# Optimization experiments

Hardware: AMD Instinct MI355X
Metric: run time of the kernel (lower is better)

## Reference

```python
import jax, jax.numpy as jnp
import numpy as np

N = 4096
IN_DIM, HID, OUT_DIM = 512, 256, 64
PROP_STEP = 10
LAM_HAT = 0.9
SCAD_A = 3.7
EPS = 1e-8


def setup_inputs() -> dict:
    key = jax.random.key(0)
    kA, kF, k1, k2 = jax.random.split(key, 4)
    # sparse symmetric 0/1 adjacency, zero diagonal (add_loops adds I later)
    u = jax.random.uniform(kA, (N, N), dtype=jnp.float32)
    A = (u < 0.005).astype(jnp.float32)
    A = jnp.maximum(A, A.T)
    A = A * (1.0 - jnp.eye(N, dtype=jnp.float32))
    F = jax.random.normal(kF, (N, IN_DIM), dtype=jnp.float32)
    W1 = jax.random.normal(k1, (IN_DIM, HID), dtype=jnp.float32) / np.sqrt(IN_DIM)
    b1 = jnp.zeros((HID,), dtype=jnp.float32)
    W2 = jax.random.normal(k2, (HID, OUT_DIM), dtype=jnp.float32) / np.sqrt(HID)
    b2 = jnp.zeros((OUT_DIM,), dtype=jnp.float32)
    raw_gamma = jnp.zeros((PROP_STEP,), dtype=jnp.float32)
    return {"A": A, "F": F, "W1": W1, "b1": b1, "W2": W2, "b2": b2,
            "raw_gamma": raw_gamma}


def reference(A, F, W1, b1, W2, b2, raw_gamma):
    lam = 1.0 / LAM_HAT - 1.0
    a = SCAD_A
    # MLP (dropout inactive at inference)
    F0 = jax.nn.relu(F @ W1 + b1) @ W2 + b2            # [N, out_dim]
    eye = jnp.eye(A.shape[0], dtype=A.dtype)
    A = A + eye                                        # add_loops
    D = A.sum(-1)                                      # [N]
    D_sq = jnp.sqrt(D)[:, None]                        # [N, 1]
    A_tilde = A / D_sq / D_sq.T                        # sym_norm: D^-1/2 A D^-1/2
    gammas = jax.nn.sigmoid(raw_gamma) * 2.0           # per-layer gamma in (0, 2)

    def step(Fc, gamma_k):
        Fn = Fc / D_sq
        nrm = jnp.linalg.norm(Fn, axis=-1, keepdims=True)
        Fu = Fn / jnp.maximum(nrm, 1e-12)
        # cosine distance in [0, 2]; detached as in torch (.detach())
        y = jax.lax.stop_gradient(1.0 - Fu @ Fu.T)     # [N, N]
        lam_k = jnp.maximum(gamma_k / a, EPS)
        t = a * lam_k
        safe_y = jnp.where(y <= 0.0, 1.0, y)
        w_mid = (t - y) / ((a - 1.0) * safe_y)
        # SCAD weight: 1 for y<=lam_k, linear decay on [lam_k, a*lam_k], 0 beyond
        W = jnp.where(y <= lam_k, 1.0, jnp.where(y <= t, w_mid, 0.0))
        W = W * (1.0 - eye)
        W = jnp.where(jnp.isnan(W), 1.0, W)
        Q_hat = ((W * A).sum(-1) / D + lam)[:, None]   # [N, 1]
        F_new = (W * A_tilde) @ Fc / Q_hat + lam * F0 / Q_hat
        return F_new, None

    F_out, _ = jax.lax.scan(step, F0, gammas)
    return F_out
```

## Files before the change

kernel.cpp:

```cpp
#include <hip/hip_runtime.h>
#include <hip/hip_bf16.h>

#define N_NODES 4096
#define IN_DIM  512
#define HID_DIM 256
#define OUT_DIM 64
#define PROP_STEP 10
#define MAX_DEG 128
#define GEMM_BLOCKS 256
#define SCAN_BLOCKS 512
#define LAM_CONST (1.0f/0.9f - 1.0f)
#define SCAD_A 3.7f

__device__ __forceinline__ ushort f2bf(float f) {
    unsigned u = __float_as_uint(f);
    unsigned r = (u + 0x7FFFu + ((u >> 16) & 1u)) >> 16;
    return (ushort)r;
}
__device__ __forceinline__ unsigned pack2(float lo, float hi) {
    return (unsigned)f2bf(lo) | ((unsigned)f2bf(hi) << 16);
}
__device__ __forceinline__ float bflo(unsigned u) { return __uint_as_float(u << 16); }
__device__ __forceinline__ float bfhi(unsigned u) { return __uint_as_float(u & 0xFFFF0000u); }
__device__ __forceinline__ float4 f4add(float4 a, float4 b) {
    return make_float4(a.x + b.x, a.y + b.y, a.z + b.z, a.w + b.w);
}

#define FMA16(AV, WV) \
    acc0.x = fmaf(AV.x, WV.x, acc0.x); acc0.y = fmaf(AV.x, WV.y, acc0.y); \
    acc0.z = fmaf(AV.x, WV.z, acc0.z); acc0.w = fmaf(AV.x, WV.w, acc0.w); \
    acc1.x = fmaf(AV.y, WV.x, acc1.x); acc1.y = fmaf(AV.y, WV.y, acc1.y); \
    acc1.z = fmaf(AV.y, WV.z, acc1.z); acc1.w = fmaf(AV.y, WV.w, acc1.w); \
    acc2.x = fmaf(AV.z, WV.x, acc2.x); acc2.y = fmaf(AV.z, WV.y, acc2.y); \
    acc2.z = fmaf(AV.z, WV.z, acc2.z); acc2.w = fmaf(AV.z, WV.w, acc2.w); \
    acc3.x = fmaf(AV.w, WV.x, acc3.x); acc3.y = fmaf(AV.w, WV.y, acc3.y); \
    acc3.z = fmaf(AV.w, WV.z, acc3.z); acc3.w = fmaf(AV.w, WV.w, acc3.w);

#define STEP(KK, WV) { float4 a_ = *(const float4*)&sF[(KK) * 16 + rg4]; FMA16(a_, WV); }

#define P2ROW(HV, PV) \
    PV.x = fmaf(HV.x, w0.x, PV.x); PV.y = fmaf(HV.x, w0.y, PV.y); \
    PV.z = fmaf(HV.x, w0.z, PV.z); PV.w = fmaf(HV.x, w0.w, PV.w); \
    PV.x = fmaf(HV.y, w1.x, PV.x); PV.y = fmaf(HV.y, w1.y, PV.y); \
    PV.z = fmaf(HV.y, w1.z, PV.z); PV.w = fmaf(HV.y, w1.w, PV.w); \
    PV.x = fmaf(HV.z, w2.x, PV.x); PV.y = fmaf(HV.z, w2.y, PV.y); \
    PV.z = fmaf(HV.z, w2.z, PV.z); PV.w = fmaf(HV.z, w2.w, PV.w); \
    PV.x = fmaf(HV.w, w3.x, PV.x); PV.y = fmaf(HV.w, w3.y, PV.y); \
    PV.z = fmaf(HV.w, w3.z, PV.z); PV.w = fmaf(HV.w, w3.w, PV.w);

__global__ __launch_bounds__(256, 4) void build_all(
    const float* __restrict__ A, const float* __restrict__ F,
    const float* __restrict__ W1, const float* __restrict__ b1,
    const float* __restrict__ W2, const float* __restrict__ b2,
    float* __restrict__ F0,
    int* __restrict__ ell, int* __restrict__ deg,
    float* __restrict__ invD, float* __restrict__ invDsq)
{
    __shared__ float smem[8192];
    if (blockIdx.x >= SCAN_BLOCKS) {
        float* sF = smem;
        int t  = threadIdx.x;
        int m0 = (blockIdx.x - SCAN_BLOCKS) * 16;
        {
            int r = t & 15, kc = (t >> 4) * 32;
            const float* src = F + (size_t)(m0 + r) * IN_DIM + kc;
#pragma unroll
            for (int j = 0; j < 8; j++) {
                float4 v = *(const float4*)(src + j * 4);
                sF[(kc + j * 4 + 0) * 16 + r] = v.x;
                sF[(kc + j * 4 + 1) * 16 + r] = v.y;
                sF[(kc + j * 4 + 2) * 16 + r] = v.z;
                sF[(kc + j * 4 + 3) * 16 + r] = v.w;
            }
        }
        __syncthreads();
        int rg4 = (t >> 6) * 4;
        int cg  = t & 63;
        const float* Wp = W1 + cg * 4;
        float4 acc0 = {0,0,0,0}, acc1 = {0,0,0,0}, acc2 = {0,0,0,0}, acc3 = {0,0,0,0};
        float4 wa0 = *(const float4*)(Wp + 0 * HID_DIM);
        float4 wa1 = *(const float4*)(Wp + 1 * HID_DIM);
        float4 wa2 = *(const float4*)(Wp + 2 * HID_DIM);
        float4 wa3 = *(const float4*)(Wp + 3 * HID_DIM);
        float4 wb0 = *(const float4*)(Wp + 4 * HID_DIM);
        float4 wb1 = *(const float4*)(Wp + 5 * HID_DIM);
        float4 wb2 = *(const float4*)(Wp + 6 * HID_DIM);
        float4 wb3 = *(const float4*)(Wp + 7 * HID_DIM);
        for (int kb = 0; kb < IN_DIM; kb += 8) {
            STEP(kb + 0, wa0) STEP(kb + 1, wa1) STEP(kb + 2, wa2) STEP(kb + 3, wa3)
            if (kb + 8 < IN_DIM) {
                const float* wn = Wp + (size_t)(kb + 8) * HID_DIM;
                wa0 = *(const float4*)(wn);
                wa1 = *(const float4*)(wn + HID_DIM);
                wa2 = *(const float4*)(wn + 2 * HID_DIM);
                wa3 = *(const float4*)(wn + 3 * HID_DIM);
            }
            STEP(kb + 4, wb0) STEP(kb + 5, wb1) STEP(kb + 6, wb2) STEP(kb + 7, wb3)
            if (kb + 8 < IN_DIM) {
                const float* wn = Wp + (size_t)(kb + 12) * HID_DIM;
                wb0 = *(const float4*)(wn);
                wb1 = *(const float4*)(wn + HID_DIM);
                wb2 = *(const float4*)(wn + 2 * HID_DIM);
                wb3 = *(const float4*)(wn + 3 * HID_DIM);
            }
        }
        __syncthreads();
        float* sH   = smem;
        float* sRed = smem + 4096;
        {
            float4 bv = *(const float4*)(b1 + cg * 4);
            float4 h0 = make_float4(fmaxf(acc0.x + bv.x, 0.f), fmaxf(acc0.y + bv.y, 0.f),
                                    fmaxf(acc0.z + bv.z, 0.f), fmaxf(acc0.w + bv.w, 0.f));
            float4 h1 = make_float4(fmaxf(acc1.x + bv.x, 0.f), fmaxf(acc1.y + bv.y, 0.f),
                                    fmaxf(acc1.z + bv.z, 0.f), fmaxf(acc1.w + bv.w, 0.f));
            float4 h2 = make_float4(fmaxf(acc2.x + bv.x, 0.f), fmaxf(acc2.y + bv.y, 0.f),
                                    fmaxf(acc2.z + bv.z, 0.f), fmaxf(acc2.w + bv.w, 0.f));
            float4 h3 = make_float4(fmaxf(acc3.x + bv.x, 0.f), fmaxf(acc3.y + bv.y, 0.f),
                                    fmaxf(acc3.z + bv.z, 0.f), fmaxf(acc3.w + bv.w, 0.f));
            *(float4*)&sH[(rg4 + 0) * 256 + cg * 4] = h0;
            *(float4*)&sH[(rg4 + 1) * 256 + cg * 4] = h1;
            *(float4*)&sH[(rg4 + 2) * 256 + cg * 4] = h2;
            *(float4*)&sH[(rg4 + 3) * 256 + cg * 4] = h3;
        }
        __syncthreads();
        int lane = t & 63, wid = t >> 6;
        int rgrp = lane >> 4;
        int cg2  = lane & 15;
        float4 p0 = {0,0,0,0}, p1 = {0,0,0,0}, p2 = {0,0,0,0}, p3 = {0,0,0,0};
        int kbase = wid * 64;
        for (int kq = 0; kq < 64; kq += 4) {
            int kg = kbase + kq;
            float4 h0 = *(const float4*)&sH[(rgrp * 4 + 0) * 256 + kg];
            float4 h1 = *(const float4*)&sH[(rgrp * 4 + 1) * 256 + kg];
            float4 h2 = *(const float4*)&sH[(rgrp * 4 + 2) * 256 + kg];
            float4 h3 = *(const float4*)&sH[(rgrp * 4 + 3) * 256 + kg];
            float4 w0 = *(const float4*)(W2 + (size_t)(kg + 0) * OUT_DIM + cg2 * 4);
            float4 w1 = *(const float4*)(W2 + (size_t)(kg + 1) * OUT_DIM + cg2 * 4);
            float4 w2 = *(const float4*)(W2 + (size_t)(kg + 2) * OUT_DIM + cg2 * 4);
            float4 w3 = *(const float4*)(W2 + (size_t)(kg + 3) * OUT_DIM + cg2 * 4);
            P2ROW(h0, p0) P2ROW(h1, p1) P2ROW(h2, p2) P2ROW(h3, p3)
        }
        __syncthreads();
        if (wid) {
            float* dst = sRed + (size_t)(wid - 1) * 1024 + lane * 16;
            *(float4*)(dst + 0)  = p0; *(float4*)(dst + 4)  = p1;
            *(float4*)(dst + 8)  = p2; *(float4*)(dst + 12) = p3;
        }
        __syncthreads();
        if (wid == 0) {
#pragma unroll
            for (int w = 0; w < 3; w++) {
                const float* s = sRed + (size_t)w * 1024 + lane * 16;
                p0 = f4add(p0, *(const float4*)(s + 0));
                p1 = f4add(p1, *(const float4*)(s + 4));
                p2 = f4add(p2, *(const float4*)(s + 8));
                p3 = f4add(p3, *(const float4*)(s + 12));
            }
            float4 b2v = *(const float4*)(b2 + cg2 * 4);
            float* o = F0 + (size_t)(m0 + rgrp * 4) * OUT_DIM + cg2 * 4;
            *(float4*)(o + 0 * OUT_DIM) = f4add(p0, b2v);
            *(float4*)(o + 1 * OUT_DIM) = f4add(p1, b2v);
            *(float4*)(o + 2 * OUT_DIM) = f4add(p2, b2v);
            *(float4*)(o + 3 * OUT_DIM) = f4add(p3, b2v);
        }
    } else {
        int sb   = blockIdx.x;
        int lane = threadIdx.x & 63;
        int wid  = threadIdx.x >> 6;
        int w    = sb * 4 + wid;
        for (int rr = 0; rr < 2; rr++) {
            int row = w * 2 + rr;
            const float* Arow = A + (size_t)row * N_NODES;
            float4 ch[16];
#pragma unroll
            for (int c = 0; c < 16; c++)
                ch[c] = *(const float4*)(Arow + c * 256 + lane * 4);
            int* rdst = ell + (size_t)row * MAX_DEG;
            unsigned cnt = 0;
#pragma unroll
            for (int c = 0; c < 16; c++) {
                float4 v = ch[c];
                int colbase = c * 256 + lane * 4;
#pragma unroll
                for (int q = 0; q < 4; q++) {
                    float vv = (q == 0) ? v.x : (q == 1) ? v.y : (q == 2) ? v.z : v.w;
                    bool nz = (vv != 0.0f);
                    unsigned long long m = __ballot(nz);
                    unsigned rank = __builtin_amdgcn_mbcnt_hi(
                        (unsigned)(m >> 32),
                        __builtin_amdgcn_mbcnt_lo((unsigned)m, 0u));
                    unsigned pos = cnt + rank;
                    if (nz && pos < MAX_DEG) rdst[pos] = colbase + q;
                    cnt += (unsigned)__popcll(m);
                }
            }
            int c  = (cnt > MAX_DEG) ? MAX_DEG : (int)cnt;
            int pad = (c + 15) & ~15;
            if (pad > MAX_DEG) pad = MAX_DEG;
            if (lane >= c && lane < pad) rdst[lane] = row;
            int l2 = lane + 64;
            if (l2 >= c && l2 < pad) rdst[l2] = row;
            if (lane == 0) {
                deg[row] = c;
                float d = (float)(cnt + 1);
                invD[row] = 1.0f / d;
                invDsq[row] = rsqrtf(d);
            }
        }
    }
}

__global__ __launch_bounds__(256, 4) void propagate_f0(
    const float* __restrict__ F0,
    const int* __restrict__ ell, const int* __restrict__ deg,
    const float* __restrict__ invD, const float* __restrict__ invDsq,
    const float* __restrict__ raw_gamma,
    unsigned* __restrict__ Pout, float* __restrict__ nrmOut)
{
    int lane = threadIdx.x & 63;
    int wid  = threadIdx.x >> 6;
    int r    = __builtin_amdgcn_readfirstlane(blockIdx.x * 4 + wid);
    int g    = lane >> 3;
    int sl   = lane & 7;
    const float inv_am1 = 1.0f / (SCAD_A - 1.0f);

    float gamma = 2.0f / (1.0f + expf(-raw_gamma[0]));
    float lam_k = fmaxf(gamma / SCAD_A, 1e-8f);
    float tt    = SCAD_A * lam_k;

    int dg = deg[r];
    int pad = (dg + 15) & ~15;
    int npair = pad >> 4;
    const int* nb = ell + (size_t)r * MAX_DEG;
    int ed0 = (lane < pad)      ? nb[lane]      : r;
    int ed1 = (64 + lane < pad) ? nb[64 + lane] : r;

    float iDs = invDsq[r];
    const float4* f04 = (const float4*)(F0 + (size_t)r * OUT_DIM + sl * 8);
    float4 fa = f04[0], fb = f04[1];
    float f0v[8] = { fa.x, fa.y, fa.z, fa.w, fb.x, fb.y, fb.z, fb.w };
    float ui[8];
    float ssr = 0.0f;
#pragma unroll
    for (int q = 0; q < 8; q++) { ui[q] = f0v[q] * iDs; ssr += ui[q] * ui[q]; }
    ssr += __shfl_xor(ssr, 1, 64);
    ssr += __shfl_xor(ssr, 2, 64);
    ssr += __shfl_xor(ssr, 4, 64);
    float inv_nr = 1.0f / fmaxf(sqrtf(ssr), 1e-12f);
#pragma unroll
    for (int q = 0; q < 8; q++) ui[q] *= inv_nr;

    float acc[8] = {};
    float qsum = 0.0f;
    for (int it = 0; it < npair; ++it) {
        int e0 = it * 16 + g, e1 = e0 + 8;
        int src = (it < 4) ? ed0 : ed1;
        int j0 = __shfl(src, e0 & 63, 64);
        int j1 = __shfl(src, e1 & 63, 64);
        const float4* p0 = (const float4*)(F0 + (size_t)j0 * OUT_DIM + sl * 8);
        const float4* p1 = (const float4*)(F0 + (size_t)j1 * OUT_DIM + sl * 8);
        float4 x0 = p0[0], x1 = p0[1];
        float4 y0 = p1[0], y1 = p1[1];
        float d0 = invDsq[j0], d1 = invDsq[j1];
        float v0[8] = { x0.x*d0, x0.y*d0, x0.z*d0, x0.w*d0, x1.x*d0, x1.y*d0, x1.z*d0, x1.w*d0 };
        float v1[8] = { y0.x*d1, y0.y*d1, y0.z*d1, y0.w*d1, y1.x*d1, y1.y*d1, y1.z*d1, y1.w*d1 };
        float pa = 0.f, pb = 0.f, s0 = 0.f, s1 = 0.f;
#pragma unroll
        for (int q = 0; q < 8; q++) {
            pa += ui[q] * v0[q]; s0 += v0[q] * v0[q];
            pb += ui[q] * v1[q]; s1 += v1[q] * v1[q];
        }
        pa += __shfl_xor(pa, 1, 64); pb += __shfl_xor(pb, 1, 64);
        s0 += __shfl_xor(s0, 1, 64); s1 += __shfl_xor(s1, 1, 64);
        pa += __shfl_xor(pa, 2, 64); pb += __shfl_xor(pb, 2, 64);
        s0 += __shfl_xor(s0, 2, 64); s1 += __shfl_xor(s1, 2, 64);
        pa += __shfl_xor(pa, 4, 64); pb += __shfl_xor(pb, 4, 64);
        s0 += __shfl_xor(s0, 4, 64); s1 += __shfl_xor(s1, 4, 64);
        float n0 = fmaxf(sqrtf(s0), 1e-12f);
        float n1 = fmaxf(sqrtf(s1), 1e-12f);
        float ya = 1.0f - pa / n0, yb = 1.0f - pb / n1;
        float wa = (ya <= lam_k) ? 1.0f : ((ya <= tt) ? (tt - ya) * inv_am1 / ya : 0.0f);
        float wb = (yb <= lam_k) ? 1.0f : ((yb <= tt) ? (tt - yb) * inv_am1 / yb : 0.0f);
        if (e0 >= dg) wa = 0.0f;
        if (e1 >= dg) wb = 0.0f;
        qsum += wa + wb;
#pragma unroll
        for (int q = 0; q < 8; q++) acc[q] += wa * v0[q] + wb * v1[q];
    }

#pragma unroll
    for (int off = 8; off <= 32; off <<= 1) {
#pragma unroll
        for (int q = 0; q < 8; q++) acc[q] += __shfl_xor(acc[q], off, 64);
        qsum += __shfl_xor(qsum, off, 64);
    }

    float Qh  = qsum * invD[r] + LAM_CONST;
    float rQh = 1.0f / Qh;
    float res[8], fn[8];
    float ssq = 0.0f;
#pragma unroll
    for (int q = 0; q < 8; q++) {
        res[q] = (acc[q] * iDs + LAM_CONST * f0v[q]) * rQh;
        fn[q]  = res[q] * iDs;
        ssq   += fn[q] * fn[q];
    }
    ssq += __shfl_xor(ssq, 1, 64);
    ssq += __shfl_xor(ssq, 2, 64);
    ssq += __shfl_xor(ssq, 4, 64);
    float nrm = fmaxf(sqrtf(ssq), 1e-12f);
    float inv_n = 1.0f / nrm;
    if (lane < 8) {
        uint4 fuPk;
        fuPk.x = pack2(fn[0] * inv_n, fn[1] * inv_n);
        fuPk.y = pack2(fn[2] * inv_n, fn[3] * inv_n);
        fuPk.z = pack2(fn[4] * inv_n, fn[5] * inv_n);
        fuPk.w = pack2(fn[6] * inv_n, fn[7] * inv_n);
        *(uint4*)(Pout + (size_t)r * 32 + sl * 4) = fuPk;
    }
    if (lane == 0) nrmOut[r] = nrm;
}

__global__ __launch_bounds__(256, 4) void propagate(
    const unsigned* __restrict__ Pin, const float* __restrict__ nrmIn,
    const float* __restrict__ F0,
    const int* __restrict__ ell, const int* __restrict__ deg,
    const float* __restrict__ invD, const float* __restrict__ invDsq,
    const float* __restrict__ raw_gamma, int step,
    unsigned* __restrict__ Pout, float* __restrict__ nrmOut,
    float* __restrict__ FcOut, int writeNext, int writeOut)
{
    int lane = threadIdx.x & 63;
    int wid  = threadIdx.x >> 6;
    int r    = __builtin_amdgcn_readfirstlane(blockIdx.x * 4 + wid);
    int g    = lane >> 3;
    int sl   = lane & 7;
    const float inv_am1 = 1.0f / (SCAD_A - 1.0f);

    float gamma = 2.0f / (1.0f + expf(-raw_gamma[step]));
    float lam_k = fmaxf(gamma / SCAD_A, 1e-8f);
    float tt    = SCAD_A * lam_k;

    int dg = deg[r];
    int pad = (dg + 15) & ~15;
    int npair = pad >> 4;
    const int* nb = ell + (size_t)r * MAX_DEG;
    int ed0 = (lane < pad)      ? nb[lane]      : r;
    int ed1 = (64 + lane < pad) ? nb[64 + lane] : r;

    uint4 up = *(const uint4*)(Pin + (size_t)r * 32 + sl * 4);
    float ui[8] = { bflo(up.x), bfhi(up.x), bflo(up.y), bfhi(up.y),
                    bflo(up.z), bfhi(up.z), bflo(up.w), bfhi(up.w) };

    float acc[8] = {};
    float qsum = 0.0f;

    auto eidx = [&](int it_, int& J0, int& J1) {
        int e0_ = it_ * 16 + g;
        int src = (it_ < 4) ? ed0 : ed1;
        J0 = __shfl(src, e0_ & 63, 64);
        J1 = __shfl(src, (e0_ + 8) & 63, 64);
    };
    auto body = [&](int it_, uint4 U0, uint4 U1, float NR0, float NR1) {
        float pa = ui[0] * bflo(U0.x) + ui[1] * bfhi(U0.x) + ui[2] * bflo(U0.y) + ui[3] * bfhi(U0.y)
                 + ui[4] * bflo(U0.z) + ui[5] * bfhi(U0.z) + ui[6] * bflo(U0.w) + ui[7] * bfhi(U0.w);
        float pb = ui[0] * bflo(U1.x) + ui[1] * bfhi(U1.x) + ui[2] * bflo(U1.y) + ui[3] * bfhi(U1.y)
                 + ui[4] * bflo(U1.z) + ui[5] * bfhi(U1.z) + ui[6] * bflo(U1.w) + ui[7] * bfhi(U1.w);
        pa += __shfl_xor(pa, 1, 64); pb += __shfl_xor(pb, 1, 64);
        pa += __shfl_xor(pa, 2, 64); pb += __shfl_xor(pb, 2, 64);
        pa += __shfl_xor(pa, 4, 64); pb += __shfl_xor(pb, 4, 64);
        float ya = 1.0f - pa, yb = 1.0f - pb;
        float wa = (ya <= lam_k) ? 1.0f : ((ya <= tt) ? (tt - ya) * inv_am1 / ya : 0.0f);
        float wb = (yb <= lam_k) ? 1.0f : ((yb <= tt) ? (tt - yb) * inv_am1 / yb : 0.0f);
        int e0_ = it_ * 16 + g;
        if (e0_ >= dg)     wa = 0.0f;
        if (e0_ + 8 >= dg) wb = 0.0f;
        qsum += wa + wb;
        float wsa = wa * NR0;
        float wsb = wb * NR1;
        acc[0] += wsa * bflo(U0.x) + wsb * bflo(U1.x);
        acc[1] += wsa * bfhi(U0.x) + wsb * bfhi(U1.x);
        acc[2] += wsa * bflo(U0.y) + wsb * bflo(U1.y);
        acc[3] += wsa * bfhi(U0.y) + wsb * bfhi(U1.y);
        acc[4] += wsa * bflo(U0.z) + wsb * bflo(U1.z);
        acc[5] += wsa * bfhi(U0.z) + wsb * bfhi(U1.z);
        acc[6] += wsa * bflo(U0.w) + wsb * bflo(U1.w);
        acc[7] += wsa * bfhi(U0.w) + wsb * bfhi(U1.w);
    };

    if (npair > 0) {
        uint4 uA0, uA1, uB0, uB1;
        float nA0, nA1, nB0, nB1;
        int j0, j1;
        eidx(0, j0, j1);
        uA0 = *(const uint4*)(Pin + (size_t)j0 * 32 + sl * 4);
        uA1 = *(const uint4*)(Pin + (size_t)j1 * 32 + sl * 4);
        nA0 = nrmIn[j0]; nA1 = nrmIn[j1];
        int it = 0;
        while (true) {
            if (it + 1 < npair) {
                eidx(it + 1, j0, j1);
                uB0 = *(const uint4*)(Pin + (size_t)j0 * 32 + sl * 4);
                uB1 = *(const uint4*)(Pin + (size_t)j1 * 32 + sl * 4);
                nB0 = nrmIn[j0]; nB1 = nrmIn[j1];
            }
            body(it, uA0, uA1, nA0, nA1);
            ++it; if (it >= npair) break;
            if (it + 1 < npair) {
                eidx(it + 1, j0, j1);
                uA0 = *(const uint4*)(Pin + (size_t)j0 * 32 + sl * 4);
                uA1 = *(const uint4*)(Pin + (size_t)j1 * 32 + sl * 4);
                nA0 = nrmIn[j0]; nA1 = nrmIn[j1];
            }
            body(it, uB0, uB1, nB0, nB1);
            ++it; if (it >= npair) break;
        }
    }

#pragma unroll
    for (int off = 8; off <= 32; off <<= 1) {
#pragma unroll
        for (int q = 0; q < 8; q++) acc[q] += __shfl_xor(acc[q], off, 64);
        qsum += __shfl_xor(qsum, off, 64);
    }

    float iDs = invDsq[r];
    float Qh  = qsum * invD[r] + LAM_CONST;
    float rQh = 1.0f / Qh;
    const float4* f04 = (const float4*)(F0 + (size_t)r * OUT_DIM + sl * 8);
    float4 f0a = f04[0], f0b = f04[1];
    float f0v[8] = { f0a.x, f0a.y, f0a.z, f0a.w, f0b.x, f0b.y, f0b.z, f0b.w };
    float res[8];
#pragma unroll
    for (int q = 0; q < 8; q++) res[q] = (acc[q] * iDs + LAM_CONST * f0v[q]) * rQh;

    if (writeOut && lane < 8) {
        float4* o4 = (float4*)(FcOut + (size_t)r * OUT_DIM + sl * 8);
        o4[0] = make_float4(res[0], res[1], res[2], res[3]);
        o4[1] = make_float4(res[4], res[5], res[6], res[7]);
    }
    if (writeNext) {
        float fn[8];
        float ssq = 0.0f;
#pragma unroll
        for (int q = 0; q < 8; q++) { fn[q] = res[q] * iDs; ssq += fn[q] * fn[q]; }
        ssq += __shfl_xor(ssq, 1, 64);
        ssq += __shfl_xor(ssq, 2, 64);
        ssq += __shfl_xor(ssq, 4, 64);
        float nrm = fmaxf(sqrtf(ssq), 1e-12f);
        float inv_n = 1.0f / nrm;
        if (lane < 8) {
            uint4 fuPk;
            fuPk.x = pack2(fn[0] * inv_n, fn[1] * inv_n);
            fuPk.y = pack2(fn[2] * inv_n, fn[3] * inv_n);
            fuPk.z = pack2(fn[4] * inv_n, fn[5] * inv_n);
            fuPk.w = pack2(fn[6] * inv_n, fn[7] * inv_n);
            *(uint4*)(Pout + (size_t)r * 32 + sl * 4) = fuPk;
        }
        if (lane == 0) nrmOut[r] = nrm;
    }
}

extern "C" void kernel_launch(void* const* d_in, const int* in_sizes, int n_in,
                              void* d_out, int out_size, void* d_ws, size_t ws_size,
                              hipStream_t stream)
{
    const float* A  = (const float*)d_in[0];
    const float* F  = (const float*)d_in[1];
    const float* W1 = (const float*)d_in[2];
    const float* b1 = (const float*)d_in[3];
    const float* W2 = (const float*)d_in[4];
    const float* b2 = (const float*)d_in[5];
    const float* rg = (const float*)d_in[6];
    float* out = (float*)d_out;

    char* p = (char*)d_ws;
    float* F0     = (float*)p; p += (size_t)N_NODES * OUT_DIM * 4;
    unsigned* Pa  = (unsigned*)p; p += (size_t)N_NODES * 32 * 4;
    unsigned* Pb  = (unsigned*)p; p += (size_t)N_NODES * 32 * 4;
    float* nrmA   = (float*)p; p += (size_t)N_NODES * 4;
    float* nrmB   = (float*)p; p += (size_t)N_NODES * 4;
    float* invD   = (float*)p; p += (size_t)N_NODES * 4;
    float* invDsq = (float*)p; p += (size_t)N_NODES * 4;
    int*   deg    = (int*)p;   p += (size_t)N_NODES * 4;
    int*   ell    = (int*)p;   p += (size_t)N_NODES * MAX_DEG * 4;

    build_all<<<GEMM_BLOCKS + SCAN_BLOCKS, 256, 0, stream>>>(
        A, F, W1, b1, W2, b2, F0, ell, deg, invD, invDsq);

    propagate_f0<<<N_NODES / 4, 256, 0, stream>>>(
        F0, ell, deg, invD, invDsq, rg, Pa, nrmA);

    for (int k = 1; k < PROP_STEP; k++) {
        unsigned* Pin   = (k & 1) ? Pa : Pb;
        unsigned* Pout  = (k & 1) ? Pb : Pa;
        float* nIn      = (k & 1) ? nrmA : nrmB;
        float* nOut     = (k & 1) ? nrmB : nrmA;
        int last = (k == PROP_STEP - 1);
        propagate<<<N_NODES / 4, 256, 0, stream>>>(
            Pin, nIn, F0, ell, deg, invD, invDsq, rg, k,
            Pout, nOut, out, !last, last);
    }
}
```

Measured before the change: 215.5 us.

## Split MLP GEMM K-dimension across waves with 8-row tiles and smem reduction

Each MLP block now handles 8 rows instead of 16, doubling the GEMM block count. Each of the four waves computes a partial product over its own 128-wide K slice and keeps 8x4 accumulators per thread. The partials are reduced in shared memory before bias and ReLU. This exposes more parallelism in the build kernel's MLP part. The cost is an extra reduction pass and syncs, and W1/W2 are reread by twice as many blocks.

Result: faster. 195.5 us (-9.3%).

```diff
diff --git a/kernel.cpp b/kernel.cpp
--- a/kernel.cpp
+++ b/kernel.cpp
@@ -7,7 +7,7 @@
 #define OUT_DIM 64
 #define PROP_STEP 10
 #define MAX_DEG 128
-#define GEMM_BLOCKS 256
+#define GEMM_BLOCKS 512
 #define SCAN_BLOCKS 512
 #define LAM_CONST (1.0f/0.9f - 1.0f)
 #define SCAD_A 3.7f
@@ -26,17 +26,28 @@
     return make_float4(a.x + b.x, a.y + b.y, a.z + b.z, a.w + b.w);
 }
 
-#define FMA16(AV, WV) \
-    acc0.x = fmaf(AV.x, WV.x, acc0.x); acc0.y = fmaf(AV.x, WV.y, acc0.y); \
-    acc0.z = fmaf(AV.x, WV.z, acc0.z); acc0.w = fmaf(AV.x, WV.w, acc0.w); \
-    acc1.x = fmaf(AV.y, WV.x, acc1.x); acc1.y = fmaf(AV.y, WV.y, acc1.y); \
-    acc1.z = fmaf(AV.y, WV.z, acc1.z); acc1.w = fmaf(AV.y, WV.w, acc1.w); \
-    acc2.x = fmaf(AV.z, WV.x, acc2.x); acc2.y = fmaf(AV.z, WV.y, acc2.y); \
-    acc2.z = fmaf(AV.z, WV.z, acc2.z); acc2.w = fmaf(AV.z, WV.w, acc2.w); \
-    acc3.x = fmaf(AV.w, WV.x, acc3.x); acc3.y = fmaf(AV.w, WV.y, acc3.y); \
-    acc3.z = fmaf(AV.w, WV.z, acc3.z); acc3.w = fmaf(AV.w, WV.w, acc3.w);
-
-#define STEP(KK, WV) { float4 a_ = *(const float4*)&sF[(KK) * 16 + rg4]; FMA16(a_, WV); }
+#define FMA32(A0, A1, WV) \
+    ac0.x = fmaf(A0.x, WV.x, ac0.x); ac0.y = fmaf(A0.x, WV.y, ac0.y); \
+    ac0.z = fmaf(A0.x, WV.z, ac0.z); ac0.w = fmaf(A0.x, WV.w, ac0.w); \
+    ac1.x = fmaf(A0.y, WV.x, ac1.x); ac1.y = fmaf(A0.y, WV.y, ac1.y); \
+    ac1.z = fmaf(A0.y, WV.z, ac1.z); ac1.w = fmaf(A0.y, WV.w, ac1.w); \
+    ac2.x = fmaf(A0.z, WV.x, ac2.x); ac2.y = fmaf(A0.z, WV.y, ac2.y); \
+    ac2.z = fmaf(A0.z, WV.z, ac2.z); ac2.w = fmaf(A0.z, WV.w, ac2.w); \
+    ac3.x = fmaf(A0.w, WV.x, ac3.x); ac3.y = fmaf(A0.w, WV.y, ac3.y); \
+    ac3.z = fmaf(A0.w, WV.z, ac3.z); ac3.w = fmaf(A0.w, WV.w, ac3.w); \
+    ac4.x = fmaf(A1.x, WV.x, ac4.x); ac4.y = fmaf(A1.x, WV.y, ac4.y); \
+    ac4.z = fmaf(A1.x, WV.z, ac4.z); ac4.w = fmaf(A1.x, WV.w, ac4.w); \
+    ac5.x = fmaf(A1.y, WV.x, ac5.x); ac5.y = fmaf(A1.y, WV.y, ac5.y); \
+    ac5.z = fmaf(A1.y, WV.z, ac5.z); ac5.w = fmaf(A1.y, WV.w, ac5.w); \
+    ac6.x = fmaf(A1.z, WV.x, ac6.x); ac6.y = fmaf(A1.z, WV.y, ac6.y); \
+    ac6.z = fmaf(A1.z, WV.z, ac6.z); ac6.w = fmaf(A1.z, WV.w, ac6.w); \
+    ac7.x = fmaf(A1.w, WV.x, ac7.x); ac7.y = fmaf(A1.w, WV.y, ac7.y); \
+    ac7.z = fmaf(A1.w, WV.z, ac7.z); ac7.w = fmaf(A1.w, WV.w, ac7.w);
+
+#define CONS(KK, WV) { \
+    float4 a0_ = *(const float4*)&sF[(KK) * 8];     \
+    float4 a1_ = *(const float4*)&sF[(KK) * 8 + 4]; \
+    FMA32(a0_, a1_, WV) }
 
 #define P2ROW(HV, PV) \
     PV.x = fmaf(HV.x, w0.x, PV.x); PV.y = fmaf(HV.x, w0.y, PV.y); \
@@ -59,25 +70,27 @@
     __shared__ float smem[8192];
     if (blockIdx.x >= SCAN_BLOCKS) {
         float* sF = smem;
-        int t  = threadIdx.x;
-        int m0 = (blockIdx.x - SCAN_BLOCKS) * 16;
+        int t    = threadIdx.x;
+        int lane = t & 63, wid = t >> 6;
+        int m0   = (blockIdx.x - SCAN_BLOCKS) * 8;
         {
-            int r = t & 15, kc = (t >> 4) * 32;
+            int r = t & 7, kc = (t >> 3) * 16;
             const float* src = F + (size_t)(m0 + r) * IN_DIM + kc;
 #pragma unroll
-            for (int j = 0; j < 8; j++) {
+            for (int j = 0; j < 4; j++) {
                 float4 v = *(const float4*)(src + j * 4);
-                sF[(kc + j * 4 + 0) * 16 + r] = v.x;
-                sF[(kc + j * 4 + 1) * 16 + r] = v.y;
-                sF[(kc + j * 4 + 2) * 16 + r] = v.z;
-                sF[(kc + j * 4 + 3) * 16 + r] = v.w;
+                sF[(kc + j * 4 + 0) * 8 + r] = v.x;
+                sF[(kc + j * 4 + 1) * 8 + r] = v.y;
+                sF[(kc + j * 4 + 2) * 8 + r] = v.z;
+                sF[(kc + j * 4 + 3) * 8 + r] = v.w;
             }
         }
         __syncthreads();
-        int rg4 = (t >> 6) * 4;
-        int cg  = t & 63;
-        const float* Wp = W1 + cg * 4;
-        float4 acc0 = {0,0,0,0}, acc1 = {0,0,0,0}, acc2 = {0,0,0,0}, acc3 = {0,0,0,0};
+        int cg = lane;
+        int kw = wid * 128;
+        const float* Wp = W1 + (size_t)kw * HID_DIM + cg * 4;
+        float4 ac0 = {0,0,0,0}, ac1 = {0,0,0,0}, ac2 = {0,0,0,0}, ac3 = {0,0,0,0};
+        float4 ac4 = {0,0,0,0}, ac5 = {0,0,0,0}, ac6 = {0,0,0,0}, ac7 = {0,0,0,0};
         float4 wa0 = *(const float4*)(Wp + 0 * HID_DIM);
         float4 wa1 = *(const float4*)(Wp + 1 * HID_DIM);
         float4 wa2 = *(const float4*)(Wp + 2 * HID_DIM);
@@ -86,17 +99,18 @@
         float4 wb1 = *(const float4*)(Wp + 5 * HID_DIM);
         float4 wb2 = *(const float4*)(Wp + 6 * HID_DIM);
         float4 wb3 = *(const float4*)(Wp + 7 * HID_DIM);
-        for (int kb = 0; kb < IN_DIM; kb += 8) {
-            STEP(kb + 0, wa0) STEP(kb + 1, wa1) STEP(kb + 2, wa2) STEP(kb + 3, wa3)
-            if (kb + 8 < IN_DIM) {
+        for (int kb = 0; kb < 128; kb += 8) {
+            int k0 = kw + kb;
+            CONS(k0 + 0, wa0) CONS(k0 + 1, wa1) CONS(k0 + 2, wa2) CONS(k0 + 3, wa3)
+            if (kb + 8 < 128) {
                 const float* wn = Wp + (size_t)(kb + 8) * HID_DIM;
                 wa0 = *(const float4*)(wn);
                 wa1 = *(const float4*)(wn + HID_DIM);
                 wa2 = *(const float4*)(wn + 2 * HID_DIM);
                 wa3 = *(const float4*)(wn + 3 * HID_DIM);
             }
-            STEP(kb + 4, wb0) STEP(kb + 5, wb1) STEP(kb + 6, wb2) STEP(kb + 7, wb3)
-            if (kb + 8 < IN_DIM) {
+            CONS(k0 + 4, wb0) CONS(k0 + 5, wb1) CONS(k0 + 6, wb2) CONS(k0 + 7, wb3)
+            if (kb + 8 < 128) {
                 const float* wn = Wp + (size_t)(kb + 12) * HID_DIM;
                 wb0 = *(const float4*)(wn);
                 wb1 = *(const float4*)(wn + HID_DIM);
@@ -105,63 +119,57 @@
             }
         }
         __syncthreads();
-        float* sH   = smem;
-        float* sRed = smem + 4096;
         {
-            float4 bv = *(const float4*)(b1 + cg * 4);
-            float4 h0 = make_float4(fmaxf(acc0.x + bv.x, 0.f), fmaxf(acc0.y + bv.y, 0.f),
-                                    fmaxf(acc0.z + bv.z, 0.f), fmaxf(acc0.w + bv.w, 0.f));
-            float4 h1 = make_float4(fmaxf(acc1.x + bv.x, 0.f), fmaxf(acc1.y + bv.y, 0.f),
-                                    fmaxf(acc1.z + bv.z, 0.f), fmaxf(acc1.w + bv.w, 0.f));
-            float4 h2 = make_float4(fmaxf(acc2.x + bv.x, 0.f), fmaxf(acc2.y + bv.y, 0.f),
-                                    fmaxf(acc2.z + bv.z, 0.f), fmaxf(acc2.w + bv.w, 0.f));
-            float4 h3 = make_float4(fmaxf(acc3.x + bv.x, 0.f), fmaxf(acc3.y + bv.y, 0.f),
-                                    fmaxf(acc3.z + bv.z, 0.f), fmaxf(acc3.w + bv.w, 0.f));
-            *(float4*)&sH[(rg4 + 0) * 256 + cg * 4] = h0;
-            *(float4*)&sH[(rg4 + 1) * 256 + cg * 4] = h1;
-            *(float4*)&sH[(rg4 + 2) * 256 + cg * 4] = h2;
-            *(float4*)&sH[(rg4 + 3) * 256 + cg * 4] = h3;
+            float* pp = smem + (size_t)wid * 2048;
+            *(float4*)&pp[0 * 256 + cg * 4] = ac0;
+            *(float4*)&pp[1 * 256 + cg * 4] = ac1;
+            *(float4*)&pp[2 * 256 + cg * 4] = ac2;
+            *(float4*)&pp[3 * 256 + cg * 4] = ac3;
+            *(float4*)&pp[4 * 256 + cg * 4] = ac4;
+            *(float4*)&pp[5 * 256 + cg * 4] = ac5;
+            *(float4*)&pp[6 * 256 + cg * 4] = ac6;
+            *(float4*)&pp[7 * 256 + cg * 4] = ac7;
         }
         __syncthreads();
-        int lane = t & 63, wid = t >> 6;
+        for (int i = t; i < 2048; i += 256) {
+            float h = smem[i] + smem[i + 2048] + smem[i + 4096] + smem[i + 6144]
+                    + b1[i & 255];
+            smem[i] = fmaxf(h, 0.0f);
+        }
+        __syncthreads();
+        float* sH = smem;
         int rgrp = lane >> 4;
         int cg2  = lane & 15;
-        float4 p0 = {0,0,0,0}, p1 = {0,0,0,0}, p2 = {0,0,0,0}, p3 = {0,0,0,0};
+        float4 p0 = {0,0,0,0}, p1 = {0,0,0,0};
         int kbase = wid * 64;
         for (int kq = 0; kq < 64; kq += 4) {
             int kg = kbase + kq;
-            float4 h0 = *(const float4*)&sH[(rgrp * 4 + 0) * 256 + kg];
-            float4 h1 = *(const float4*)&sH[(rgrp * 4 + 1) * 256 + kg];
-            float4 h2 = *(const float4*)&sH[(rgrp * 4 + 2) * 256 + kg];
-            float4 h3 = *(const float4*)&sH[(rgrp * 4 + 3) * 256 + kg];
+            float4 h0 = *(const float4*)&sH[(rgrp * 2 + 0) * 256 + kg];
+            float4 h1 = *(const float4*)&sH[(rgrp * 2 + 1) * 256 + kg];
             float4 w0 = *(const float4*)(W2 + (size_t)(kg + 0) * OUT_DIM + cg2 * 4);
             float4 w1 = *(const float4*)(W2 + (size_t)(kg + 1) * OUT_DIM + cg2 * 4);
             float4 w2 = *(const float4*)(W2 + (size_t)(kg + 2) * OUT_DIM + cg2 * 4);
             float4 w3 = *(const float4*)(W2 + (size_t)(kg + 3) * OUT_DIM + cg2 * 4);
-            P2ROW(h0, p0) P2ROW(h1, p1) P2ROW(h2, p2) P2ROW(h3, p3)
+            P2ROW(h0, p0) P2ROW(h1, p1)
         }
         __syncthreads();
         if (wid) {
-            float* dst = sRed + (size_t)(wid - 1) * 1024 + lane * 16;
-            *(float4*)(dst + 0)  = p0; *(float4*)(dst + 4)  = p1;
-            *(float4*)(dst + 8)  = p2; *(float4*)(dst + 12) = p3;
+            float* dst = smem + 2048 + (size_t)(wid - 1) * 512 + lane * 8;
+            *(float4*)(dst + 0) = p0;
+            *(float4*)(dst + 4) = p1;
         }
         __syncthreads();
         if (wid == 0) {
 #pragma unroll
             for (int w = 0; w < 3; w++) {
-                const float* s = sRed + (size_t)w * 1024 + lane * 16;
+                const float* s = smem + 2048 + (size_t)w * 512 + lane * 8;
                 p0 = f4add(p0, *(const float4*)(s + 0));
                 p1 = f4add(p1, *(const float4*)(s + 4));
-                p2 = f4add(p2, *(const float4*)(s + 8));
-                p3 = f4add(p3, *(const float4*)(s + 12));
             }
             float4 b2v = *(const float4*)(b2 + cg2 * 4);
-            float* o = F0 + (size_t)(m0 + rgrp * 4) * OUT_DIM + cg2 * 4;
+            float* o = F0 + (size_t)(m0 + rgrp * 2) * OUT_DIM + cg2 * 4;
             *(float4*)(o + 0 * OUT_DIM) = f4add(p0, b2v);
             *(float4*)(o + 1 * OUT_DIM) = f4add(p1, b2v);
-            *(float4*)(o + 2 * OUT_DIM) = f4add(p2, b2v);
-            *(float4*)(o + 3 * OUT_DIM) = f4add(p3, b2v);
         }
     } else {
         int sb   = blockIdx.x;
```
